# Kernel optimization log

Hardware: AMD Instinct MI355X
Metric: run time of the kernel (lower is better)

The kernel has to match this reference:

```python
import jax, jax.numpy as jnp
import numpy as np

B, S, D, H, F, L = 4, 2048, 768, 12, 3072, 4
DH = D // H  # dim_head = 64
EPS = 1e-5


def _layernorm(x, g, b):
    mu = jnp.mean(x, axis=-1, keepdims=True)
    var = jnp.var(x, axis=-1, keepdims=True)
    return (x - mu) * jax.lax.rsqrt(var + EPS) * g + b


def setup_inputs() -> dict:
    key = jax.random.key(0)
    ks = jax.random.split(key, 12)
    sc = 0.02
    x = jax.random.normal(ks[0], (B, S, D), dtype=jnp.float32)
    # causal mask: True where attention is disallowed (j > i)
    causal = jnp.triu(jnp.ones((S, S), dtype=bool), k=1)
    attn_mask = jnp.broadcast_to(causal, (B, S, S))
    Wq = jax.random.normal(ks[1], (L, D, D), dtype=jnp.float32) * sc
    Wk = jax.random.normal(ks[2], (L, D, D), dtype=jnp.float32) * sc
    Wv = jax.random.normal(ks[3], (L, D, D), dtype=jnp.float32) * sc
    Wo = jax.random.normal(ks[4], (L, D, D), dtype=jnp.float32) * sc
    bo = jnp.zeros((L, D), dtype=jnp.float32)
    ln1_g = jnp.ones((L, D), dtype=jnp.float32)
    ln1_b = jnp.zeros((L, D), dtype=jnp.float32)
    W1 = jax.random.normal(ks[5], (L, D, F), dtype=jnp.float32) * sc
    b1 = jnp.zeros((L, F), dtype=jnp.float32)
    W2 = jax.random.normal(ks[6], (L, F, D), dtype=jnp.float32) * sc
    b2 = jnp.zeros((L, D), dtype=jnp.float32)
    ln2_g = jnp.ones((L, D), dtype=jnp.float32)
    ln2_b = jnp.zeros((L, D), dtype=jnp.float32)
    return dict(x=x, attn_mask=attn_mask, Wq=Wq, Wk=Wk, Wv=Wv, Wo=Wo, bo=bo,
                ln1_g=ln1_g, ln1_b=ln1_b, W1=W1, b1=b1, W2=W2, b2=b2,
                ln2_g=ln2_g, ln2_b=ln2_b)


def _decoder_layer(x, mask, Wq, Wk, Wv, Wo, bo, ln1_g, ln1_b, W1, b1, W2, b2, ln2_g, ln2_b):
    # multi-head attention (dropout = identity in eval)
    q = (x @ Wq).reshape(B, S, H, DH).transpose(0, 2, 1, 3)  # (B,H,S,DH)
    k = (x @ Wk).reshape(B, S, H, DH).transpose(0, 2, 1, 3)
    v = (x @ Wv).reshape(B, S, H, DH).transpose(0, 2, 1, 3)
    a = jnp.einsum('bhqd,bhkd->bhqk', q, k) / jnp.sqrt(jnp.float32(DH))
    a = jnp.where(mask[:, None, :, :], jnp.float32(-1e9), a)
    p = jax.nn.softmax(a, axis=-1)
    av = jnp.einsum('bhqk,bhkd->bhqd', p, v)
    av = av.transpose(0, 2, 1, 3).reshape(B, S, D)
    attn_out = av @ Wo + bo
    h = _layernorm(x + attn_out, ln1_g, ln1_b)
    # FFN: Conv1d(kernel=1) == pointwise linear; exact GELU (torch F.gelu default)
    f = jax.nn.gelu(h @ W1 + b1, approximate=False) @ W2 + b2
    return _layernorm(h + f, ln2_g, ln2_b)


def reference(x, attn_mask, Wq, Wk, Wv, Wo, bo, ln1_g, ln1_b, W1, b1, W2, b2, ln2_g, ln2_b):
    for l in range(L):
        x = _decoder_layer(x, attn_mask, Wq[l], Wk[l], Wv[l], Wo[l], bo[l],
                           ln1_g[l], ln1_b[l], W1[l], b1[l], W2[l], b2[l],
                           ln2_g[l], ln2_b[l])
    return x
```

## Files before the change

### kernel.cpp

```cpp
#include <hip/hip_runtime.h>
#include <hip/hip_bf16.h>
#include <math.h>

#define BB 4
#define SS 2048
#define DD 768
#define HH 12
#define DHD 64
#define FF 3072
#define LL 4

typedef float f4 __attribute__((ext_vector_type(4)));
typedef float ffrag __attribute__((ext_vector_type(4)));
typedef __bf16 bf16x8 __attribute__((ext_vector_type(8)));
typedef __bf16 bf16x4 __attribute__((ext_vector_type(4)));

__device__ __forceinline__ void gld_lds16(const __bf16* g, __bf16* l) {
  __builtin_amdgcn_global_load_lds(
      (const __attribute__((address_space(1))) void*)g,
      (__attribute__((address_space(3))) void*)l, 16, 0, 0);
}

template <int ACT, int WRITE_BF16, int QKV>
__global__ __launch_bounds__(256) void gemm_mfma(
    const __bf16* __restrict__ A,
    const __bf16* __restrict__ Bt,
    const float* __restrict__ bias,
    float* __restrict__ Cf,
    __bf16* __restrict__ Cb,
    __bf16* __restrict__ Vt,
    int M, int N, int K) {
  __shared__ __bf16 As[128 * 64];
  __shared__ __bf16 Bs[128 * 64];
  const int tid = threadIdx.x;
  const int lane = tid & 63;
  const int wid = tid >> 6;
  const int m0 = blockIdx.y * 128;
  const int n0 = blockIdx.x * 128;
  const int wm = (wid >> 1) * 64;
  const int wn = (wid & 1) * 64;

  ffrag acc[4][4];
#pragma unroll
  for (int i = 0; i < 4; ++i)
#pragma unroll
    for (int j = 0; j < 4; ++j) acc[i][j] = (ffrag)0.f;

  const int kr = lane >> 4;
  const int ml = lane & 15;

  for (int k0 = 0; k0 < K; k0 += 64) {
    __syncthreads();
#pragma unroll
    for (int it = 0; it < 4; ++it) {
      const int gidx = it * 256 + wid * 64 + lane;
      const int row = gidx >> 3;
      const int gl = (gidx & 7) ^ (row & 7);
      gld_lds16(A + (size_t)(m0 + row) * K + k0 + gl * 8,
                As + (size_t)(it * 256 + wid * 64) * 8);
      gld_lds16(Bt + (size_t)(n0 + row) * K + k0 + gl * 8,
                Bs + (size_t)(it * 256 + wid * 64) * 8);
    }
    __syncthreads();

#pragma unroll
    for (int kh = 0; kh < 64; kh += 32) {
      const int gb = (kh >> 3) + kr;
      bf16x8 af[4], bfr[4];
#pragma unroll
      for (int i = 0; i < 4; ++i) {
        const int ra = wm + i * 16 + ml;
        af[i] = *(const bf16x8*)(As + ra * 64 + ((gb ^ (ra & 7)) * 8));
        const int rb = wn + i * 16 + ml;
        bfr[i] = *(const bf16x8*)(Bs + rb * 64 + ((gb ^ (rb & 7)) * 8));
      }
#pragma unroll
      for (int i = 0; i < 4; ++i)
#pragma unroll
        for (int j = 0; j < 4; ++j)
          acc[i][j] = __builtin_amdgcn_mfma_f32_16x16x32_bf16(
              af[i], bfr[j], acc[i][j], 0, 0, 0);
    }
  }

  const int rq = (lane >> 4) * 4;
#pragma unroll
  for (int j = 0; j < 4; ++j) {
    const int col = n0 + wn + j * 16 + ml;
    const float bv = (!QKV && bias) ? bias[col] : 0.f;
#pragma unroll
    for (int i = 0; i < 4; ++i) {
      const int row = m0 + wm + i * 16 + rq;
      if (QKV) {
        if (col < 1536) {
#pragma unroll
          for (int r = 0; r < 4; ++r)
            Cb[(size_t)(row + r) * 1536 + col] = (__bf16)acc[i][j][r];
        } else {
          const int df = col - 1536;
          const int hh = df >> 6, d = df & 63;
          const int bi = row >> 11, s = row & 2047;
          bf16x4 pk;
#pragma unroll
          for (int r = 0; r < 4; ++r) pk[r] = (__bf16)acc[i][j][r];
          *(bf16x4*)(Vt + ((size_t)(bi * HH + hh) * DHD + d) * SS + s) = pk;
        }
      } else {
#pragma unroll
        for (int r = 0; r < 4; ++r) {
          float v = acc[i][j][r] + bv;
          if (ACT) v = 0.5f * v * (1.f + erff(v * 0.70710678118654752f));
          if (WRITE_BF16)
            Cb[(size_t)(row + r) * N + col] = (__bf16)v;
          else
            Cf[(size_t)(row + r) * N + col] = v;
        }
      }
    }
  }
}

__global__ __launch_bounds__(256) void wtrans_kernel(
    const float* __restrict__ src, __bf16* __restrict__ dst, int R, int C,
    size_t src_ls, size_t dst_ls) {
  __shared__ float t[32][33];
  src += (size_t)blockIdx.z * src_ls;
  dst += (size_t)blockIdx.z * dst_ls;
  const int tx = threadIdx.x & 31;
  const int ty = threadIdx.x >> 5;
  const int r0 = blockIdx.y * 32;
  const int c0 = blockIdx.x * 32;
#pragma unroll
  for (int i = 0; i < 4; ++i)
    t[ty + i * 8][tx] = src[(size_t)(r0 + ty + i * 8) * C + c0 + tx];
  __syncthreads();
#pragma unroll
  for (int i = 0; i < 4; ++i)
    dst[(size_t)(c0 + ty + i * 8) * R + r0 + tx] = (__bf16)t[tx][ty + i * 8];
}

__global__ __launch_bounds__(256) void cvt_kernel(
    const float* __restrict__ x, __bf16* __restrict__ y, int n4) {
  const int i = blockIdx.x * 256 + threadIdx.x;
  if (i < n4) {
    const float4 v = *(const float4*)(x + (size_t)i * 4);
    bf16x4 o;
    o[0] = (__bf16)v.x; o[1] = (__bf16)v.y;
    o[2] = (__bf16)v.z; o[3] = (__bf16)v.w;
    *(bf16x4*)(y + (size_t)i * 4) = o;
  }
}

__global__ __launch_bounds__(256, 4) void attn_mfma(
    const __bf16* __restrict__ QK, const __bf16* __restrict__ VT,
    __bf16* __restrict__ O) {
  __shared__ __bf16 qs[64 * 64];
  __shared__ __bf16 ks[64 * 64];
  __shared__ __bf16 vts[64 * 64];
  __shared__ __bf16 ps[64 * 72];

  const int h = blockIdx.y;
  const int b = blockIdx.z;
  const int tid = threadIdx.x;
  const int lane = tid & 63;
  const int wid = tid >> 6;
  const int ml = lane & 15;
  const int quad = lane >> 4;
  const int wq = wid * 16;
  const size_t rowbase = (size_t)b * SS;
  const int hc = h * 64;
  const size_t vbase = (size_t)(b * HH + h) * DHD;
  const int NT = SS / 64;

  for (int ph = 0; ph < 2; ++ph) {
    const int qt = ph ? (NT - 1 - (int)blockIdx.x) : (int)blockIdx.x;
    const int q0 = qt * 64;

    __syncthreads();
#pragma unroll
    for (int it = 0; it < 2; ++it) {
      const int gidx = it * 256 + wid * 64 + lane;
      const int row = gidx >> 3;
      const int gl = (gidx & 7) ^ (row & 7);
      gld_lds16(QK + (rowbase + q0 + row) * 1536 + hc + gl * 8,
                qs + (size_t)(it * 256 + wid * 64) * 8);
    }

    ffrag oacc[4];
#pragma unroll
    for (int d = 0; d < 4; ++d) oacc[d] = (ffrag)0.f;
    float l_acc = 0.f;

    for (int ch = 0; ch <= qt; ++ch) {
      const int j0 = ch * 64;
      __syncthreads();

#pragma unroll
      for (int it = 0; it < 2; ++it) {
        const int gidx = it * 256 + wid * 64 + lane;
        const int row = gidx >> 3;
        const int gl = (gidx & 7) ^ (row & 7);
        gld_lds16(QK + (rowbase + j0 + row) * 1536 + 768 + hc + gl * 8,
                  ks + (size_t)(it * 256 + wid * 64) * 8);
        gld_lds16(VT + (vbase + row) * SS + j0 + gl * 8,
                  vts + (size_t)(it * 256 + wid * 64) * 8);
      }
      __syncthreads();

      ffrag sa[4];
#pragma unroll
      for (int jt = 0; jt < 4; ++jt) sa[jt] = (ffrag)0.f;
#pragma unroll
      for (int kk = 0; kk < 2; ++kk) {
        const int gb = kk * 4 + quad;
        const int ra = wq + ml;
        const bf16x8 qf = *(const bf16x8*)(qs + ra * 64 + ((gb ^ (ra & 7)) * 8));
#pragma unroll
        for (int jt = 0; jt < 4; ++jt) {
          const int rb = jt * 16 + ml;
          const bf16x8 kf = *(const bf16x8*)(ks + rb * 64 + ((gb ^ (rb & 7)) * 8));
          sa[jt] = __builtin_amdgcn_mfma_f32_16x16x32_bf16(kf, qf, sa[jt], 0, 0, 0);
        }
      }

      const bool maskch = (j0 == q0);
      const int qrel = wq + ml;
      float lsum = 0.f;
      bf16x4 pk[4];
#pragma unroll
      for (int jt = 0; jt < 4; ++jt) {
#pragma unroll
        for (int r = 0; r < 4; ++r) {
          float p = __expf(sa[jt][r] * 0.125f);
          if (maskch && (jt * 16 + quad * 4 + r > qrel)) p = 0.f;
          lsum += p;
          pk[jt][r] = (__bf16)p;
        }
      }
      lsum += __shfl_xor(lsum, 16);
      lsum += __shfl_xor(lsum, 32);
      l_acc += lsum;

#pragma unroll
      for (int jt = 0; jt < 4; ++jt)
        *(bf16x4*)(ps + (size_t)(wq + ml) * 72 + jt * 16 + quad * 4) = pk[jt];

#pragma unroll
      for (int kk = 0; kk < 2; ++kk) {
        const bf16x8 ap =
            *(const bf16x8*)(ps + (size_t)(wq + ml) * 72 + kk * 32 + quad * 8);
        const int gb = kk * 4 + quad;
#pragma unroll
        for (int d = 0; d < 4; ++d) {
          const int rv = d * 16 + ml;
          const bf16x8 bv =
              *(const bf16x8*)(vts + rv * 64 + ((gb ^ (rv & 7)) * 8));
          oacc[d] = __builtin_amdgcn_mfma_f32_16x16x32_bf16(ap, bv, oacc[d], 0, 0, 0);
        }
      }
    }

#pragma unroll
    for (int r = 0; r < 4; ++r) {
      const int qloc = quad * 4 + r;
      const float lr = __shfl(l_acc, qloc);
      const float inv = 1.f / lr;
      const size_t row = rowbase + q0 + wq + qloc;
#pragma unroll
      for (int d = 0; d < 4; ++d)
        O[row * DD + hc + d * 16 + ml] = (__bf16)(oacc[d][r] * inv);
    }
  }
}

__global__ __launch_bounds__(256) void add_ln_kernel(
    const float* __restrict__ X, const float* __restrict__ R,
    const float* __restrict__ g, const float* __restrict__ be,
    float* __restrict__ O, __bf16* __restrict__ Ob) {
  const int row = blockIdx.x * 4 + (threadIdx.x >> 6);
  const int lane = threadIdx.x & 63;
  const float* xr = X + (size_t)row * DD;
  const float* rr = R + (size_t)row * DD;
  float v[12];
  float sum = 0.f;
#pragma unroll
  for (int i = 0; i < 3; ++i) {
    const float4 a = *(const float4*)(xr + i * 256 + lane * 4);
    const float4 c = *(const float4*)(rr + i * 256 + lane * 4);
    v[i * 4 + 0] = a.x + c.x;
    v[i * 4 + 1] = a.y + c.y;
    v[i * 4 + 2] = a.z + c.z;
    v[i * 4 + 3] = a.w + c.w;
    sum += v[i * 4 + 0] + v[i * 4 + 1] + v[i * 4 + 2] + v[i * 4 + 3];
  }
#pragma unroll
  for (int off = 32; off >= 1; off >>= 1) sum += __shfl_xor(sum, off);
  const float mean = sum * (1.f / 768.f);
  float sq = 0.f;
#pragma unroll
  for (int i = 0; i < 12; ++i) {
    const float d = v[i] - mean;
    sq += d * d;
  }
#pragma unroll
  for (int off = 32; off >= 1; off >>= 1) sq += __shfl_xor(sq, off);
  const float inv = rsqrtf(sq * (1.f / 768.f) + 1e-5f);
#pragma unroll
  for (int i = 0; i < 3; ++i) {
    const int c = i * 256 + lane * 4;
    const float4 gg = *(const float4*)(g + c);
    const float4 bb = *(const float4*)(be + c);
    float4 o;
    o.x = (v[i * 4 + 0] - mean) * inv * gg.x + bb.x;
    o.y = (v[i * 4 + 1] - mean) * inv * gg.y + bb.y;
    o.z = (v[i * 4 + 2] - mean) * inv * gg.z + bb.z;
    o.w = (v[i * 4 + 3] - mean) * inv * gg.w + bb.w;
    *(float4*)(O + (size_t)row * DD + c) = o;
    bf16x4 ob;
    ob[0] = (__bf16)o.x; ob[1] = (__bf16)o.y;
    ob[2] = (__bf16)o.z; ob[3] = (__bf16)o.w;
    *(bf16x4*)(Ob + (size_t)row * DD + c) = ob;
  }
}

extern "C" void kernel_launch(void* const* d_in, const int* in_sizes, int n_in,
                              void* d_out, int out_size, void* d_ws,
                              size_t ws_size, hipStream_t stream) {
  const float* x0   = (const float*)d_in[0];
  const float* Wq   = (const float*)d_in[2];
  const float* Wk   = (const float*)d_in[3];
  const float* Wv   = (const float*)d_in[4];
  const float* Wo   = (const float*)d_in[5];
  const float* bo   = (const float*)d_in[6];
  const float* ln1g = (const float*)d_in[7];
  const float* ln1b = (const float*)d_in[8];
  const float* W1   = (const float*)d_in[9];
  const float* b1   = (const float*)d_in[10];
  const float* W2   = (const float*)d_in[11];
  const float* b2   = (const float*)d_in[12];
  const float* ln2g = (const float*)d_in[13];
  const float* ln2b = (const float*)d_in[14];

  float* out = (float*)d_out;

  const size_t NTD = (size_t)BB * SS * DD;
  __bf16* qkbf = (__bf16*)d_ws;
  __bf16* vtbf = qkbf + (size_t)BB * SS * 1536;
  __bf16* xbf  = vtbf + NTD;
  __bf16* midbf = qkbf;
  float* aw   = (float*)(xbf + NTD);
  float* hbuf = aw + NTD;
  __bf16* btbf = (__bf16*)(hbuf + NTD);
  __bf16* hbf  = btbf + NTD;
  __bf16* wT   = hbf + NTD;

  const size_t WTL = 7077888;
  const size_t OQK = 0, OWO = (size_t)2304 * 768, OW1 = 2359296, OW2 = 4718592;

  const int M = BB * SS;
  const size_t DSQ = (size_t)DD * DD;

  cvt_kernel<<<(int)(NTD / 4 + 255) / 256, 256, 0, stream>>>(x0, xbf, (int)(NTD / 4));

  wtrans_kernel<<<dim3(24, 24, LL), 256, 0, stream>>>(Wq, wT + OQK, DD, DD, DSQ, WTL);
  wtrans_kernel<<<dim3(24, 24, LL), 256, 0, stream>>>(Wk, wT + (size_t)768 * 768, DD, DD, DSQ, WTL);
  wtrans_kernel<<<dim3(24, 24, LL), 256, 0, stream>>>(Wv, wT + (size_t)1536 * 768, DD, DD, DSQ, WTL);
  wtrans_kernel<<<dim3(24, 24, LL), 256, 0, stream>>>(Wo, wT + OWO, DD, DD, DSQ, WTL);
  wtrans_kernel<<<dim3(96, 24, LL), 256, 0, stream>>>(W1, wT + OW1, DD, FF, (size_t)DD * FF, WTL);
  wtrans_kernel<<<dim3(24, 96, LL), 256, 0, stream>>>(W2, wT + OW2, FF, DD, (size_t)FF * DD, WTL);

  for (int l = 0; l < LL; ++l) {
    const float* xin = (l == 0) ? x0 : out;
    const float* bol = bo + (size_t)l * DD;
    const float* g1 = ln1g + (size_t)l * DD;
    const float* be1 = ln1b + (size_t)l * DD;
    const float* b1l = b1 + (size_t)l * FF;
    const float* b2l = b2 + (size_t)l * DD;
    const float* g2 = ln2g + (size_t)l * DD;
    const float* be2 = ln2b + (size_t)l * DD;
    __bf16* wqkvT = wT + l * WTL + OQK;
    __bf16* woT   = wT + l * WTL + OWO;
    __bf16* w1T   = wT + l * WTL + OW1;
    __bf16* w2T   = wT + l * WTL + OW2;

    gemm_mfma<0, 1, 1><<<dim3(18, 64), 256, 0, stream>>>(
        xbf, wqkvT, nullptr, nullptr, qkbf, vtbf, M, 2304, DD);
    attn_mfma<<<dim3(SS / 128, HH, BB), 256, 0, stream>>>(qkbf, vtbf, btbf);
    gemm_mfma<0, 0, 0><<<dim3(6, 64), 256, 0, stream>>>(
        btbf, woT, bol, aw, nullptr, nullptr, M, DD, DD);
    add_ln_kernel<<<M / 4, 256, 0, stream>>>(xin, aw, g1, be1, hbuf, hbf);
    gemm_mfma<1, 1, 0><<<dim3(24, 64), 256, 0, stream>>>(
        hbf, w1T, b1l, nullptr, midbf, nullptr, M, FF, DD);
    gemm_mfma<0, 0, 0><<<dim3(6, 64), 256, 0, stream>>>(
        midbf, w2T, b2l, aw, nullptr, nullptr, M, DD, FF);
    add_ln_kernel<<<M / 4, 256, 0, stream>>>(hbuf, aw, g2, be2, out, xbf);
  }
}
```

Baseline: 1.432 ms.

## Double-buffer attention K/V tiles, vectorize GEMM epilogues, split QKV GEMM, cheaper GELU

The attention kernel now double-buffers K and V tiles in LDS. It prefetches the next chunk while computing the current one and drops the second barrier per chunk, with occupancy lowered to 3 blocks per CU. The GEMM swaps MFMA operand order so each lane holds 4 consecutive columns, allowing vectorized bias loads and float4/bf16x4 stores. The fused QKV GEMM is split into a QK launch and a separate V-transpose launch, removing the per-column branch. The exact erf GELU is replaced by a sigmoid-based tanh approximation, which trades accuracy for cheaper math.

```diff
diff --git a/kernel.cpp b/kernel.cpp
--- a/kernel.cpp
+++ b/kernel.cpp
@@ -21,7 +21,13 @@
       (__attribute__((address_space(3))) void*)l, 16, 0, 0);
 }
 
-template <int ACT, int WRITE_BF16, int QKV>
+__device__ __forceinline__ float gelu_f(float x) {
+  const float x2 = x * x;
+  const float e = __expf(x * fmaf(-0.0713548162f, x2, -1.5957691216f));
+  return x / (1.f + e);
+}
+
+template <int ACT, int WRITE_BF16, int MODE>
 __global__ __launch_bounds__(256) void gemm_mfma(
     const __bf16* __restrict__ A,
     const __bf16* __restrict__ Bt,
@@ -48,6 +54,7 @@
 
   const int kr = lane >> 4;
   const int ml = lane & 15;
+  const int quad = lane >> 4;
 
   for (int k0 = 0; k0 < K; k0 += 64) {
     __syncthreads();
@@ -77,43 +84,63 @@
 #pragma unroll
       for (int i = 0; i < 4; ++i)
 #pragma unroll
-        for (int j = 0; j < 4; ++j)
-          acc[i][j] = __builtin_amdgcn_mfma_f32_16x16x32_bf16(
-              af[i], bfr[j], acc[i][j], 0, 0, 0);
-    }
-  }
-
-  const int rq = (lane >> 4) * 4;
-#pragma unroll
-  for (int j = 0; j < 4; ++j) {
-    const int col = n0 + wn + j * 16 + ml;
-    const float bv = (!QKV && bias) ? bias[col] : 0.f;
-#pragma unroll
-    for (int i = 0; i < 4; ++i) {
-      const int row = m0 + wm + i * 16 + rq;
-      if (QKV) {
-        if (col < 1536) {
-#pragma unroll
-          for (int r = 0; r < 4; ++r)
-            Cb[(size_t)(row + r) * 1536 + col] = (__bf16)acc[i][j][r];
+        for (int j = 0; j < 4; ++j) {
+          if (MODE == 2)
+            acc[i][j] = __builtin_amdgcn_mfma_f32_16x16x32_bf16(
+                af[i], bfr[j], acc[i][j], 0, 0, 0);
+          else
+            acc[i][j] = __builtin_amdgcn_mfma_f32_16x16x32_bf16(
+                bfr[j], af[i], acc[i][j], 0, 0, 0);
+        }
+    }
+  }
+
+  if (MODE == 2) {
+    const int rq = quad * 4;
+#pragma unroll
+    for (int j = 0; j < 4; ++j) {
+      const int col = n0 + wn + j * 16 + ml;
+      const int hh = col >> 6, d = col & 63;
+#pragma unroll
+      for (int i = 0; i < 4; ++i) {
+        const int row = m0 + wm + i * 16 + rq;
+        const int bi = row >> 11, s = row & 2047;
+        bf16x4 pk;
+#pragma unroll
+        for (int r = 0; r < 4; ++r) pk[r] = (__bf16)acc[i][j][r];
+        *(bf16x4*)(Vt + ((size_t)(bi * HH + hh) * DHD + d) * SS + s) = pk;
+      }
+    }
+  } else {
+#pragma unroll
+    for (int j = 0; j < 4; ++j) {
+      const int ncol = n0 + wn + j * 16 + quad * 4;
+      float4 b4 = make_float4(0.f, 0.f, 0.f, 0.f);
+      if (MODE == 0 && bias) b4 = *(const float4*)(bias + ncol);
+#pragma unroll
+      for (int i = 0; i < 4; ++i) {
+        const int mrow = m0 + wm + i * 16 + ml;
+        float v0 = acc[i][j][0] + b4.x;
+        float v1 = acc[i][j][1] + b4.y;
+        float v2 = acc[i][j][2] + b4.z;
+        float v3 = acc[i][j][3] + b4.w;
+        if (ACT) {
+          v0 = gelu_f(v0); v1 = gelu_f(v1);
+          v2 = gelu_f(v2); v3 = gelu_f(v3);
+        }
+        if (MODE == 1) {
+          bf16x4 pk;
+          pk[0] = (__bf16)v0; pk[1] = (__bf16)v1;
+          pk[2] = (__bf16)v2; pk[3] = (__bf16)v3;
+          *(bf16x4*)(Cb + (size_t)mrow * 1536 + ncol) = pk;
+        } else if (WRITE_BF16) {
+          bf16x4 pk;
+          pk[0] = (__bf16)v0; pk[1] = (__bf16)v1;
+          pk[2] = (__bf16)v2; pk[3] = (__bf16)v3;
+          *(bf16x4*)(Cb + (size_t)mrow * N + ncol) = pk;
         } else {
-          const int df = col - 1536;
-          const int hh = df >> 6, d = df & 63;
-          const int bi = row >> 11, s = row & 2047;
-          bf16x4 pk;
-#pragma unroll
-          for (int r = 0; r < 4; ++r) pk[r] = (__bf16)acc[i][j][r];
-          *(bf16x4*)(Vt + ((size_t)(bi * HH + hh) * DHD + d) * SS + s) = pk;
-        }
-      } else {
-#pragma unroll
-        for (int r = 0; r < 4; ++r) {
-          float v = acc[i][j][r] + bv;
-          if (ACT) v = 0.5f * v * (1.f + erff(v * 0.70710678118654752f));
-          if (WRITE_BF16)
-            Cb[(size_t)(row + r) * N + col] = (__bf16)v;
-          else
-            Cf[(size_t)(row + r) * N + col] = v;
+          float4 o; o.x = v0; o.y = v1; o.z = v2; o.w = v3;
+          *(float4*)(Cf + (size_t)mrow * N + ncol) = o;
         }
       }
     }
@@ -151,12 +178,12 @@
   }
 }
 
-__global__ __launch_bounds__(256, 4) void attn_mfma(
+__global__ __launch_bounds__(256, 3) void attn_mfma(
     const __bf16* __restrict__ QK, const __bf16* __restrict__ VT,
     __bf16* __restrict__ O) {
   __shared__ __bf16 qs[64 * 64];
-  __shared__ __bf16 ks[64 * 64];
-  __shared__ __bf16 vts[64 * 64];
+  __shared__ __bf16 ks[2][64 * 64];
+  __shared__ __bf16 vts[2][64 * 64];
   __shared__ __bf16 ps[64 * 72];
 
   const int h = blockIdx.y;
@@ -172,19 +199,29 @@
   const size_t vbase = (size_t)(b * HH + h) * DHD;
   const int NT = SS / 64;
 
+  const int gidx0 = wid * 64 + lane;
+  const int row0 = gidx0 >> 3;
+  const int gl0 = (gidx0 & 7) ^ (row0 & 7);
+  const int gidx1 = 256 + wid * 64 + lane;
+  const int row1 = gidx1 >> 3;
+  const int gl1 = (gidx1 & 7) ^ (row1 & 7);
+
   for (int ph = 0; ph < 2; ++ph) {
     const int qt = ph ? (NT - 1 - (int)blockIdx.x) : (int)blockIdx.x;
     const int q0 = qt * 64;
 
     __syncthreads();
-#pragma unroll
-    for (int it = 0; it < 2; ++it) {
-      const int gidx = it * 256 + wid * 64 + lane;
-      const int row = gidx >> 3;
-      const int gl = (gidx & 7) ^ (row & 7);
-      gld_lds16(QK + (rowbase + q0 + row) * 1536 + hc + gl * 8,
-                qs + (size_t)(it * 256 + wid * 64) * 8);
-    }
+
+    gld_lds16(QK + (rowbase + q0 + row0) * 1536 + hc + gl0 * 8,
+              qs + (size_t)(wid * 64) * 8);
+    gld_lds16(QK + (rowbase + q0 + row1) * 1536 + hc + gl1 * 8,
+              qs + (size_t)(256 + wid * 64) * 8);
+    gld_lds16(QK + (rowbase + row0) * 1536 + 768 + hc + gl0 * 8,
+              ks[0] + (size_t)(wid * 64) * 8);
+    gld_lds16(QK + (rowbase + row1) * 1536 + 768 + hc + gl1 * 8,
+              ks[0] + (size_t)(256 + wid * 64) * 8);
+    gld_lds16(VT + (vbase + row0) * SS + gl0 * 8, vts[0] + (size_t)(wid * 64) * 8);
+    gld_lds16(VT + (vbase + row1) * SS + gl1 * 8, vts[0] + (size_t)(256 + wid * 64) * 8);
 
     ffrag oacc[4];
 #pragma unroll
@@ -193,19 +230,20 @@
 
     for (int ch = 0; ch <= qt; ++ch) {
       const int j0 = ch * 64;
+      const int cur = ch & 1;
       __syncthreads();
 
-#pragma unroll
-      for (int it = 0; it < 2; ++it) {
-        const int gidx = it * 256 + wid * 64 + lane;
-        const int row = gidx >> 3;
-        const int gl = (gidx & 7) ^ (row & 7);
-        gld_lds16(QK + (rowbase + j0 + row) * 1536 + 768 + hc + gl * 8,
-                  ks + (size_t)(it * 256 + wid * 64) * 8);
-        gld_lds16(VT + (vbase + row) * SS + j0 + gl * 8,
-                  vts + (size_t)(it * 256 + wid * 64) * 8);
-      }
-      __syncthreads();
+      if (ch < qt) {
+        const int jn = j0 + 64;
+        gld_lds16(QK + (rowbase + jn + row0) * 1536 + 768 + hc + gl0 * 8,
+                  ks[cur ^ 1] + (size_t)(wid * 64) * 8);
+        gld_lds16(QK + (rowbase + jn + row1) * 1536 + 768 + hc + gl1 * 8,
+                  ks[cur ^ 1] + (size_t)(256 + wid * 64) * 8);
+        gld_lds16(VT + (vbase + row0) * SS + jn + gl0 * 8,
+                  vts[cur ^ 1] + (size_t)(wid * 64) * 8);
+        gld_lds16(VT + (vbase + row1) * SS + jn + gl1 * 8,
+                  vts[cur ^ 1] + (size_t)(256 + wid * 64) * 8);
+      }
 
       ffrag sa[4];
 #pragma unroll
@@ -218,7 +256,8 @@
 #pragma unroll
         for (int jt = 0; jt < 4; ++jt) {
           const int rb = jt * 16 + ml;
-          const bf16x8 kf = *(const bf16x8*)(ks + rb * 64 + ((gb ^ (rb & 7)) * 8));
+          const bf16x8 kf =
+              *(const bf16x8*)(ks[cur] + rb * 64 + ((gb ^ (rb & 7)) * 8));
           sa[jt] = __builtin_amdgcn_mfma_f32_16x16x32_bf16(kf, qf, sa[jt], 0, 0, 0);
         }
       }
@@ -254,7 +293,7 @@
         for (int d = 0; d < 4; ++d) {
           const int rv = d * 16 + ml;
           const bf16x8 bv =
-              *(const bf16x8*)(vts + rv * 64 + ((gb ^ (rv & 7)) * 8));
+              *(const bf16x8*)(vts[cur] + rv * 64 + ((gb ^ (rv & 7)) * 8));
           oacc[d] = __builtin_amdgcn_mfma_f32_16x16x32_bf16(ap, bv, oacc[d], 0, 0, 0);
         }
       }
@@ -383,8 +422,11 @@
     __bf16* w1T   = wT + l * WTL + OW1;
     __bf16* w2T   = wT + l * WTL + OW2;
 
-    gemm_mfma<0, 1, 1><<<dim3(18, 64), 256, 0, stream>>>(
-        xbf, wqkvT, nullptr, nullptr, qkbf, vtbf, M, 2304, DD);
+    gemm_mfma<0, 1, 1><<<dim3(12, 64), 256, 0, stream>>>(
+        xbf, wqkvT, nullptr, nullptr, qkbf, nullptr, M, 1536, DD);
+    gemm_mfma<0, 0, 2><<<dim3(6, 64), 256, 0, stream>>>(
+        xbf, wqkvT + (size_t)1536 * 768, nullptr, nullptr, nullptr, vtbf,
+        M, 768, DD);
     attn_mfma<<<dim3(SS / 128, HH, BB), 256, 0, stream>>>(qkbf, vtbf, btbf);
     gemm_mfma<0, 0, 0><<<dim3(6, 64), 256, 0, stream>>>(
         btbf, woT, bol, aw, nullptr, nullptr, M, DD, DD);
```

New measurement: 1.367 ms. 4.5% less time.
